# Kernel optimization log

Hardware: AMD Instinct MI355X
Metric: run time of the kernel (lower is better)

The kernel has to match this reference:

```python
import jax, jax.numpy as jnp
import numpy as np

HIDDEN = 1024
NUM_HEAD = 16
HEAD_DIM = HIDDEN // NUM_HEAD
VOCAB = 32000
MAX_LEN = 1024
EMBED = 512
BATCH = 4
SEQ = MAX_LEN  # mask broadcasting requires seq == max_len


def setup_inputs() -> dict:
    key = jax.random.key(0)
    ks = jax.random.split(key, 12)
    std = 0.02
    inp = {
        'input_ids': jax.random.randint(ks[0], (BATCH, SEQ), 0, VOCAB),
        'W_word': jax.random.normal(ks[1], (VOCAB, EMBED), jnp.float32) * std,
        'W_pos': jax.random.normal(ks[2], (MAX_LEN, EMBED), jnp.float32) * std,
        'Wq': jax.random.normal(ks[3], (HIDDEN, HIDDEN), jnp.float32) * std,
        'Wk': jax.random.normal(ks[4], (HIDDEN, HIDDEN), jnp.float32) * std,
        'Wv': jax.random.normal(ks[5], (HIDDEN, HIDDEN), jnp.float32) * std,
        'Wo': jax.random.normal(ks[6], (HIDDEN, HIDDEN), jnp.float32) * std,
        'W1': jax.random.normal(ks[7], (4 * HIDDEN, HIDDEN), jnp.float32) * std,
        'W2': jax.random.normal(ks[8], (HIDDEN, 4 * HIDDEN), jnp.float32) * std,
        'W_eh': jax.random.normal(ks[9], (HIDDEN, EMBED), jnp.float32) * std,
        'W_he': jax.random.normal(ks[10], (EMBED, HIDDEN), jnp.float32) * std,
        'W_lm': jax.random.normal(ks[11], (VOCAB, EMBED), jnp.float32) * std,
    }
    return inp


def reference(input_ids, W_word, W_pos, Wq, Wk, Wv, Wo, W1, W2, W_eh, W_he, W_lm):
    B, S = input_ids.shape
    # embeddings
    h = W_word[input_ids] + W_pos[jnp.arange(S)][None, :, :]  # [B,S,E]
    h = h @ W_eh.T  # embed -> hidden, [B,S,H]
    residual = h
    # QKV projections (Linear with weight [out,in]: y = x @ W.T)
    q = (h @ Wq.T).reshape(B, S, NUM_HEAD, HEAD_DIM).transpose(0, 2, 1, 3)
    k = (h @ Wk.T).reshape(B, S, NUM_HEAD, HEAD_DIM).transpose(0, 2, 1, 3)
    v = (h @ Wv.T).reshape(B, S, NUM_HEAD, HEAD_DIM).transpose(0, 2, 1, 3)
    # note: original scales by sqrt(hidden_size), NOT sqrt(head_dim)
    scores = jnp.einsum('bhqd,bhkd->bhqk', q, k) / jnp.sqrt(jnp.float32(HIDDEN))
    mask = jnp.tril(jnp.ones((S, S), dtype=bool))[None, None]
    scores = jnp.where(mask, scores, jnp.finfo(jnp.float32).min)
    attn = jax.nn.softmax(scores.astype(jnp.float32), axis=-1)
    out = jnp.einsum('bhqk,bhkd->bhqd', attn, v)
    out = out.transpose(0, 2, 1, 3).reshape(B, S, HIDDEN)
    h = residual + out @ Wo.T
    # MLP
    residual = h
    x = jax.nn.relu(h @ W1.T)
    h = residual + x @ W2.T
    # hidden -> embed, lm head
    h = h @ W_he.T
    logits = h @ W_lm.T  # [B,S,VOCAB]
    return logits
```

## Files before the change

### kernel.cpp

```cpp
#include <hip/hip_runtime.h>
#include <hip/hip_bf16.h>

#define HIDDEN 1024
#define NHEAD 16
#define HDIM 64
#define VOCAB 32000
#define SEQLEN 1024
#define EMBED 512
#define BATCH 4
#define ROWS (BATCH*SEQLEN)

typedef __bf16 bf16x8 __attribute__((ext_vector_type(8)));
typedef float f32x4 __attribute__((ext_vector_type(4)));
typedef unsigned short u16;

#define MFMA(a_, b_, c_) __builtin_amdgcn_mfma_f32_16x16x32_bf16(a_, b_, c_, 0, 0, 0)

#define VMCNT4 asm volatile("s_waitcnt vmcnt(4)" ::: "memory")
#define VMCNT0 asm volatile("s_waitcnt vmcnt(0)" ::: "memory")
#define LGKM0  asm volatile("s_waitcnt lgkmcnt(0)" ::: "memory")
#define CFENCE asm volatile("" ::: "memory")
#define SBAR   __builtin_amdgcn_s_barrier()
#define SCHEDB __builtin_amdgcn_sched_barrier(0)

__device__ __forceinline__ u16 f2bf(float f) {
  unsigned u = __builtin_bit_cast(unsigned, f);
  u = u + 0x7FFFu + ((u >> 16) & 1u);
  return (u16)(u >> 16);
}
__device__ __forceinline__ float bf2f(u16 s) {
  unsigned u = (unsigned)s << 16;
  return __builtin_bit_cast(float, u);
}

#define GLDS(g_, l_) __builtin_amdgcn_global_load_lds( \
    (const __attribute__((address_space(1))) void*)(g_), \
    (__attribute__((address_space(3))) void*)(l_), 16, 0, 0)

struct Prep {
  const float* src[8]; u16* dst[8];
  const float* wlm; u16* wlm_dst;
  const int* ids; const float* wword; const float* wpos; u16* h0b;
};
__global__ void prep_kernel(Prep pp) {
  int b = blockIdx.x;
  if (b < 13312) {
    int seg, off;
    if (b < 4096)        { seg = b >> 10; off = b & 1023; }
    else if (b < 8192)   { seg = 4; off = b - 4096; }
    else if (b < 12288)  { seg = 5; off = b - 8192; }
    else if (b < 12800)  { seg = 6; off = b - 12288; }
    else                 { seg = 7; off = b - 12800; }
    size_t i = ((size_t)off * 256 + threadIdx.x) * 4;
    float4 v = *(const float4*)(pp.src[seg] + i);
    unsigned a = f2bf(v.x) | ((unsigned)f2bf(v.y) << 16);
    unsigned d = f2bf(v.z) | ((unsigned)f2bf(v.w) << 16);
    *(uint2*)(pp.dst[seg] + i) = make_uint2(a, d);
  } else if (b < 29312) {
    if (!pp.wlm_dst) return;
    int off = b - 13312;
    size_t i = ((size_t)off * 256 + threadIdx.x) * 4;
    float4 v = *(const float4*)(pp.wlm + i);
    unsigned a = f2bf(v.x) | ((unsigned)f2bf(v.y) << 16);
    unsigned d = f2bf(v.z) | ((unsigned)f2bf(v.w) << 16);
    *(uint2*)(pp.wlm_dst + i) = make_uint2(a, d);
  } else {
    int off = b - 29312;
    int row = off * 2 + (threadIdx.x >> 7);
    int e = (threadIdx.x & 127) * 4;
    int s = row & (SEQLEN - 1);
    int id = pp.ids[row];
    float4 a = *(const float4*)(pp.wword + (size_t)id * EMBED + e);
    float4 c = *(const float4*)(pp.wpos + (size_t)s * EMBED + e);
    unsigned lo = f2bf(a.x + c.x) | ((unsigned)f2bf(a.y + c.y) << 16);
    unsigned hi = f2bf(a.z + c.z) | ((unsigned)f2bf(a.w + c.w) << 16);
    *(uint2*)(pp.h0b + (size_t)row * EMBED + e) = make_uint2(lo, hi);
  }
}

template<int EPI, bool WF32, bool WB16, bool BF32, bool SWZ, bool NT, int BN>
__global__ __launch_bounds__(256, 2) void gemm128(
    const u16* __restrict__ A, const u16* __restrict__ Bb,
    const float* __restrict__ Bf,
    float* __restrict__ C, u16* __restrict__ Cb,
    const u16* __restrict__ R, int K, int ldc)
{
  constexpr int NF  = BN / 32;
  constexpr int BCH = BN / 32;
  __shared__ __align__(16) u16 smem[16384 + 2 * BN * 64];
  u16* As0 = &smem[0];
  u16* As1 = &smem[8192];
  u16* Bs0 = &smem[16384];
  u16* Bs1 = &smem[16384 + BN * 64];

  int tid = threadIdx.x;
  int lane = tid & 63, wave = tid >> 6;
  int wr = wave >> 1, wc = wave & 1;
  int cl = lane & 15, gp = (lane >> 4) & 3;

  int bx = blockIdx.x, by = blockIdx.y;
  if (SWZ) {
    int nwg = gridDim.x * gridDim.y;
    int flat = by * gridDim.x + bx;
    int cpx = nwg >> 3;
    int swz = (flat & 7) * cpx + (flat >> 3);
    bx = swz % gridDim.x; by = swz / gridDim.x;
  }
  int m0 = bx * 128, n0 = by * BN;

  int srow8 = lane >> 3;
  int scol = (((lane & 7) - srow8) & 7) * 8;
  int pos0 = ((gp + cl) & 7) * 8;
  int pos1 = ((gp + cl + 4) & 7) * 8;

  f32x4 acc[4][NF] = {};
  int nk = K >> 6;

  #pragma unroll
  for (int i = 0; i < 4; ++i) {
    int c = i * 4 + wave;
    GLDS(A + (size_t)(m0 + c * 8 + srow8) * K + scol, As0 + c * 512);
  }
  if (!BF32) {
    #pragma unroll
    for (int i = 0; i < BCH; ++i) {
      int c = i * 4 + wave;
      GLDS(Bb + (size_t)(n0 + c * 8 + srow8) * K + scol, Bs0 + c * 512);
    }
  } else {
    #pragma unroll
    for (int it = 0; it < BN / 32; ++it) {
      int idx = it * 256 + tid;
      int row = idx >> 3, p = idx & 7;
      int gc = (p - row) & 7;
      const float* src = Bf + (size_t)(n0 + row) * K + gc * 8;
      float4 v0 = *(const float4*)src, v1 = *(const float4*)(src + 4);
      union { bf16x8 v; u16 s[8]; } u;
      u.s[0]=f2bf(v0.x); u.s[1]=f2bf(v0.y); u.s[2]=f2bf(v0.z); u.s[3]=f2bf(v0.w);
      u.s[4]=f2bf(v1.x); u.s[5]=f2bf(v1.y); u.s[6]=f2bf(v1.z); u.s[7]=f2bf(v1.w);
      *(bf16x8*)&Bs0[row * 64 + p * 8] = u.v;
    }
  }

  for (int kt = 0; kt < nk; ++kt) {
    int buf = kt & 1;
    u16* Asb = buf ? As1 : As0;
    u16* Bsb = buf ? Bs1 : Bs0;
    u16* Asn = buf ? As0 : As1;
    u16* Bsn = buf ? Bs0 : Bs1;
    int kb = (kt + 1) << 6;
    bool more = kt + 1 < nk;

    if (more) {
      #pragma unroll
      for (int i = 0; i < 4; ++i) {
        int c = i * 4 + wave;
        GLDS(A + (size_t)(m0 + c * 8 + srow8) * K + kb + scol, Asn + c * 512);
      }
    }
    if (BF32) { VMCNT0; } else if (more) { VMCNT4; } else { VMCNT0; }
    SCHEDB;
    SBAR;
    CFENCE; SCHEDB;

    bf16x8 af[4][2], bfv[NF][2];
    #pragma unroll
    for (int n = 0; n < NF; ++n) {
      int r = (wc * (BN / 2) + n * 16 + cl) * 64;
      bfv[n][0] = *(const bf16x8*)&Bsb[r + pos0];
      bfv[n][1] = *(const bf16x8*)&Bsb[r + pos1];
    }
    #pragma unroll
    for (int m = 0; m < 4; ++m) {
      int r = (wr * 64 + m * 16 + cl) * 64;
      af[m][0] = *(const bf16x8*)&Asb[r + pos0];
      af[m][1] = *(const bf16x8*)&Asb[r + pos1];
    }

    __builtin_amdgcn_s_setprio(1);
    #pragma unroll
    for (int m = 0; m < 2; ++m)
      #pragma unroll
      for (int n = 0; n < NF; ++n)
        #pragma unroll
        for (int ks = 0; ks < 2; ++ks)
          acc[m][n] = MFMA(af[m][ks], bfv[n][ks], acc[m][n]);
    __builtin_amdgcn_s_setprio(0);

    if (more) {
      if (!BF32) {
        #pragma unroll
        for (int i = 0; i < BCH; ++i) {
          int c = i * 4 + wave;
          GLDS(Bb + (size_t)(n0 + c * 8 + srow8) * K + kb + scol, Bsn + c * 512);
        }
      } else {
        #pragma unroll
        for (int it = 0; it < BN / 32; ++it) {
          int idx = it * 256 + tid;
          int row = idx >> 3, p = idx & 7;
          int gc = (p - row) & 7;
          const float* src = Bf + (size_t)(n0 + row) * K + kb + gc * 8;
          float4 v0 = *(const float4*)src, v1 = *(const float4*)(src + 4);
          union { bf16x8 v; u16 s[8]; } u;
          u.s[0]=f2bf(v0.x); u.s[1]=f2bf(v0.y); u.s[2]=f2bf(v0.z); u.s[3]=f2bf(v0.w);
          u.s[4]=f2bf(v1.x); u.s[5]=f2bf(v1.y); u.s[6]=f2bf(v1.z); u.s[7]=f2bf(v1.w);
          *(bf16x8*)&Bsn[row * 64 + p * 8] = u.v;
        }
      }
    }

    __builtin_amdgcn_s_setprio(1);
    #pragma unroll
    for (int n = 0; n < NF; ++n)
      #pragma unroll
      for (int ks = 0; ks < 2; ++ks)
        acc[2][n] = MFMA(af[2][ks], bfv[n][ks], acc[2][n]);
    __builtin_amdgcn_s_setprio(0);

    LGKM0;
    SCHEDB;
    SBAR;
    CFENCE; SCHEDB;

    __builtin_amdgcn_s_setprio(1);
    #pragma unroll
    for (int n = 0; n < NF; ++n)
      #pragma unroll
      for (int ks = 0; ks < 2; ++ks)
        acc[3][n] = MFMA(af[3][ks], bfv[n][ks], acc[3][n]);
    __builtin_amdgcn_s_setprio(0);
  }

  if constexpr (WF32 && !WB16 && BN == 128) {
    float* Cst = (float*)&smem[0];
    __syncthreads();
    #pragma unroll
    for (int g = 0; g < 2; ++g) {
      if (wr == g) {
        #pragma unroll
        for (int m = 0; m < 4; ++m)
          #pragma unroll
          for (int n = 0; n < 4; ++n)
            #pragma unroll
            for (int j = 0; j < 4; ++j)
              Cst[(m * 16 + gp * 4 + j) * 132 + wc * 64 + n * 16 + cl] = acc[m][n][j];
      }
      __syncthreads();
      int r2 = lane >> 5, cw = lane & 31;
      #pragma unroll
      for (int p = 0; p < 8; ++p) {
        int r = p * 8 + wave * 2 + r2;
        int grow = m0 + g * 64 + r;
        f32x4 v = *(f32x4*)&Cst[r * 132 + cw * 4];
        if constexpr (EPI == 1) {
          ushort4 rv = *(const ushort4*)&R[(size_t)grow * ldc + n0 + cw * 4];
          v[0] += bf2f(rv.x); v[1] += bf2f(rv.y); v[2] += bf2f(rv.z); v[3] += bf2f(rv.w);
        }
        if constexpr (EPI == 2) {
          #pragma unroll
          for (int j = 0; j < 4; ++j) v[j] = fmaxf(v[j], 0.f);
        }
        if (NT) __builtin_nontemporal_store(v, (f32x4*)&C[(size_t)grow * ldc + n0 + cw * 4]);
        else *(f32x4*)&C[(size_t)grow * ldc + n0 + cw * 4] = v;
      }
      __syncthreads();
    }
  } else {
    int r0 = gp * 4;
    #pragma unroll
    for (int m = 0; m < 4; ++m) {
      #pragma unroll
      for (int n = 0; n < NF; ++n) {
        int col = n0 + wc * (BN / 2) + n * 16 + cl;
        #pragma unroll
        for (int j = 0; j < 4; ++j) {
          int row = m0 + wr * 64 + m * 16 + r0 + j;
          float v = acc[m][n][j];
          if (EPI == 1) v += bf2f(R[(size_t)row * ldc + col]);
          if (EPI == 2) v = fmaxf(v, 0.f);
          if (WF32) C[(size_t)row * ldc + col] = v;
          if (WB16) Cb[(size_t)row * ldc + col] = f2bf(v);
        }
      }
    }
  }
}

template<int EPI, bool WF32, bool WB16, bool SWZ, bool NT = false>
__global__ __launch_bounds__(512) void gemm256(
    const u16* __restrict__ A, const u16* __restrict__ B,
    float* __restrict__ C, u16* __restrict__ Cb,
    const u16* __restrict__ R, int K, int ldc)
{
  __shared__ __align__(16) u16 smem[4][256 * 64];
  int tid = threadIdx.x;
  int lane = tid & 63, wave = tid >> 6;
  int wr = wave >> 2, wc = wave & 3;
  int cl = lane & 15, gp = (lane >> 4) & 3;

  int bx = blockIdx.x, by = blockIdx.y;
  if (SWZ) {
    int nwg = gridDim.x * gridDim.y;
    int flat = by * gridDim.x + bx;
    int cpx = nwg >> 3;
    int swz = (flat & 7) * cpx + (flat >> 3);
    bx = swz % gridDim.x; by = swz / gridDim.x;
  }
  int m0 = bx * 256, n0 = by * 256;

  int srow8 = lane >> 3;
  int scol = (((lane & 7) - srow8) & 7) * 8;
  int pos0 = ((gp + cl) & 7) * 8;
  int pos1 = ((gp + cl + 4) & 7) * 8;

  f32x4 acc[8][4] = {};
  int nk = K >> 6;

  #pragma unroll
  for (int i = 0; i < 4; ++i) {
    int c = i * 8 + wave;
    GLDS(A + (size_t)(m0 + c * 8 + srow8) * K + scol, &smem[0][c * 512]);
  }
  #pragma unroll
  for (int i = 0; i < 4; ++i) {
    int c = i * 8 + wave;
    GLDS(B + (size_t)(n0 + c * 8 + srow8) * K + scol, &smem[2][c * 512]);
  }

  for (int kt = 0; kt < nk; ++kt) {
    int buf = kt & 1;
    int kb = (kt + 1) << 6;
    bool more = kt + 1 < nk;

    if (more) {
      #pragma unroll
      for (int i = 0; i < 4; ++i) {
        int c = i * 8 + wave;
        GLDS(A + (size_t)(m0 + c * 8 + srow8) * K + kb + scol, &smem[buf ^ 1][c * 512]);
      }
      VMCNT4;
    } else {
      VMCNT0;
    }
    SCHEDB;
    SBAR;
    CFENCE; SCHEDB;

    bf16x8 af0[4][2], af1[4][2], bf0[2][2], bf1[2][2];
    #pragma unroll
    for (int n = 0; n < 2; ++n) {
      int r = (wc * 64 + n * 16 + cl) * 64;
      bf0[n][0] = *(const bf16x8*)&smem[2 + buf][r + pos0];
      bf0[n][1] = *(const bf16x8*)&smem[2 + buf][r + pos1];
    }
    #pragma unroll
    for (int m = 0; m < 4; ++m) {
      int r = (wr * 128 + m * 16 + cl) * 64;
      af0[m][0] = *(const bf16x8*)&smem[buf][r + pos0];
      af0[m][1] = *(const bf16x8*)&smem[buf][r + pos1];
    }
    #pragma unroll
    for (int n = 0; n < 2; ++n) {
      int r = (wc * 64 + (n + 2) * 16 + cl) * 64;
      bf1[n][0] = *(const bf16x8*)&smem[2 + buf][r + pos0];
      bf1[n][1] = *(const bf16x8*)&smem[2 + buf][r + pos1];
    }
    #pragma unroll
    for (int m = 0; m < 4; ++m) {
      int r = (wr * 128 + (m + 4) * 16 + cl) * 64;
      af1[m][0] = *(const bf16x8*)&smem[buf][r + pos0];
      af1[m][1] = *(const bf16x8*)&smem[buf][r + pos1];
    }

    __builtin_amdgcn_s_setprio(1);
    #pragma unroll
    for (int m = 0; m < 4; ++m)
      #pragma unroll
      for (int n = 0; n < 2; ++n)
        #pragma unroll
        for (int ks = 0; ks < 2; ++ks)
          acc[m][n] = MFMA(af0[m][ks], bf0[n][ks], acc[m][n]);
    __builtin_amdgcn_s_setprio(0);

    if (more) {
      #pragma unroll
      for (int i = 0; i < 4; ++i) {
        int c = i * 8 + wave;
        GLDS(B + (size_t)(n0 + c * 8 + srow8) * K + kb + scol, &smem[2 + (buf ^ 1)][c * 512]);
      }
    }

    __builtin_amdgcn_s_setprio(1);
    #pragma unroll
    for (int m = 0; m < 4; ++m)
      #pragma unroll
      for (int n = 0; n < 2; ++n)
        #pragma unroll
        for (int ks = 0; ks < 2; ++ks)
          acc[m][n + 2] = MFMA(af0[m][ks], bf1[n][ks], acc[m][n + 2]);
    __builtin_amdgcn_s_setprio(0);

    LGKM0;
    SCHEDB;
    SBAR;
    CFENCE; SCHEDB;

    __builtin_amdgcn_s_setprio(1);
    #pragma unroll
    for (int m = 0; m < 4; ++m)
      #pragma unroll
      for (int n = 0; n < 2; ++n)
        #pragma unroll
        for (int ks = 0; ks < 2; ++ks)
          acc[m + 4][n] = MFMA(af1[m][ks], bf0[n][ks], acc[m + 4][n]);
    #pragma unroll
    for (int m = 0; m < 4; ++m)
      #pragma unroll
      for (int n = 0; n < 2; ++n)
        #pragma unroll
        for (int ks = 0; ks < 2; ++ks)
          acc[m + 4][n + 2] = MFMA(af1[m][ks], bf1[n][ks], acc[m + 4][n + 2]);
    __builtin_amdgcn_s_setprio(0);
  }

  if constexpr (WF32 && !WB16) {
    float* Cst = (float*)&smem[0][0];
    __syncthreads();
    #pragma unroll
    for (int g = 0; g < 4; ++g) {
      if ((g >> 1) == wr) {
        #pragma unroll
        for (int k = 0; k < 4; ++k) {
          int ar = (g & 1) * 4 + k;
          int rl = ar * 16 + gp * 4 - (g & 1) * 64;
          #pragma unroll
          for (int n = 0; n < 4; ++n) {
            int col = wc * 64 + n * 16 + cl;
            #pragma unroll
            for (int j = 0; j < 4; ++j)
              Cst[(rl + j) * 260 + col] = acc[ar][n][j];
          }
        }
      }
      __syncthreads();
      #pragma unroll
      for (int p = 0; p < 8; ++p) {
        int r = p * 8 + wave;
        int c4 = lane * 4;
        int grow = m0 + g * 64 + r;
        f32x4 v = *(f32x4*)&Cst[r * 260 + c4];
        if constexpr (EPI == 1) {
          ushort4 rv = *(const ushort4*)&R[(size_t)grow * ldc + n0 + c4];
          v[0] += bf2f(rv.x); v[1] += bf2f(rv.y); v[2] += bf2f(rv.z); v[3] += bf2f(rv.w);
        }
        if constexpr (EPI == 2) {
          #pragma unroll
          for (int j = 0; j < 4; ++j) v[j] = fmaxf(v[j], 0.f);
        }
        if (NT) __builtin_nontemporal_store(v, (f32x4*)&C[(size_t)grow * ldc + n0 + c4]);
        else *(f32x4*)&C[(size_t)grow * ldc + n0 + c4] = v;
      }
      __syncthreads();
    }
  } else {
    int r0 = gp * 4;
    #pragma unroll
    for (int m = 0; m < 8; ++m) {
      #pragma unroll
      for (int n = 0; n < 4; ++n) {
        int col = n0 + wc * 64 + n * 16 + cl;
        #pragma unroll
        for (int j = 0; j < 4; ++j) {
          int row = m0 + wr * 128 + m * 16 + r0 + j;
          float v = acc[m][n][j];
          if (EPI == 1) v += bf2f(R[(size_t)row * ldc + col]);
          if (EPI == 2) v = fmaxf(v, 0.f);
          if (WF32) C[(size_t)row * ldc + col] = v;
          if (WB16) Cb[(size_t)row * ldc + col] = f2bf(v);
        }
      }
    }
  }
}

#define LSTR 72
__global__ __launch_bounds__(256) void attn_kernel(const u16* __restrict__ qkv,
                                                   u16* __restrict__ outb) {
  __shared__ u16 Ksm[2][64 * 64];
  __shared__ u16 Vsm[2][64 * LSTR];
  __shared__ u16 Psm[64 * LSTR];
  int pi = blockIdx.x, h = blockIdx.y, b = blockIdx.z;
  int qbA = pi, qbB = 15 - pi;
  int tid = threadIdx.x;
  int lane = tid & 63, wave = tid >> 6;
  int cl = lane & 15, gp = lane >> 4;
  int srow8 = lane >> 3;
  int gsrc = (((lane & 7) - srow8) & 7) * 8;

  const u16* base = qkv + (size_t)b * SEQLEN * (3 * HIDDEN);

  bf16x8 qA0, qA1, qB0, qB1;
  {
    const u16* qp = base + (size_t)(qbA * 64 + wave * 16 + cl) * (3 * HIDDEN) + h * HDIM;
    qA0 = *(const bf16x8*)(qp + gp * 8);
    qA1 = *(const bf16x8*)(qp + 32 + gp * 8);
    const u16* qq = base + (size_t)(qbB * 64 + wave * 16 + cl) * (3 * HIDDEN) + h * HDIM;
    qB0 = *(const bf16x8*)(qq + gp * 8);
    qB1 = *(const bf16x8*)(qq + 32 + gp * 8);
  }

  ushort4 vr[4];
  auto stageK = [&](int t, int bb) {
    #pragma unroll
    for (int i = 0; i < 2; ++i) {
      int c = wave * 2 + i;
      int row = c * 8 + srow8;
      GLDS(base + (size_t)(t * 64 + row) * (3 * HIDDEN) + HIDDEN + h * HDIM + gsrc,
           &Ksm[bb][c * 512]);
    }
  };
  auto loadV = [&](int t) {
    #pragma unroll
    for (int it = 0; it < 4; ++it) {
      int idx = it * 256 + tid;
      int row = idx >> 4, c4 = (idx & 15) * 4;
      vr[it] = *(const ushort4*)(base + (size_t)(t * 64 + row) * (3 * HIDDEN) +
                                 2 * HIDDEN + h * HDIM + c4);
    }
  };
  auto writeV = [&](int bb) {
    #pragma unroll
    for (int it = 0; it < 4; ++it) {
      int idx = it * 256 + tid;
      int row = idx >> 4, c4 = (idx & 15) * 4;
      Vsm[bb][(c4 + 0) * LSTR + row] = vr[it].x;
      Vsm[bb][(c4 + 1) * LSTR + row] = vr[it].y;
      Vsm[bb][(c4 + 2) * LSTR + row] = vr[it].z;
      Vsm[bb][(c4 + 3) * LSTR + row] = vr[it].w;
    }
  };

  float mA[4], lA[4], mB[4], lB[4];
  f32x4 oA[4] = {}, oB[4] = {};
  #pragma unroll
  for (int j = 0; j < 4; ++j) { mA[j] = -INFINITY; lA[j] = 0.f; mB[j] = -INFINITY; lB[j] = 0.f; }

  auto stateStep = [&](int t, int buf, int qb, bf16x8 q0, bf16x8 q1,
                       float* mrow, float* lrow, f32x4* oacc) {
    f32x4 sfr[4];
    __builtin_amdgcn_s_setprio(1);
    #pragma unroll
    for (int n = 0; n < 4; ++n) {
      f32x4 z = {};
      bf16x8 kf0 = *(const bf16x8*)&Ksm[buf][(n * 16 + cl) * 64 + ((gp + cl) & 7) * 8];
      bf16x8 kf1 = *(const bf16x8*)&Ksm[buf][(n * 16 + cl) * 64 + ((gp + cl + 4) & 7) * 8];
      z = MFMA(q0, kf0, z);
      z = MFMA(q1, kf1, z);
      sfr[n] = z;
    }
    __builtin_amdgcn_s_setprio(0);

    bool diag = (t == qb);
    #pragma unroll
    for (int n = 0; n < 4; ++n)
      #pragma unroll
      for (int j = 0; j < 4; ++j) {
        float sv = sfr[n][j] * 0.03125f;
        if (diag) {
          int lr = wave * 16 + gp * 4 + j;
          int lc = n * 16 + cl;
          sv = (lc <= lr) ? sv : -1e30f;
        }
        sfr[n][j] = sv;
      }
    float so[4];
    #pragma unroll
    for (int j = 0; j < 4; ++j) {
      float tm = fmaxf(fmaxf(sfr[0][j], sfr[1][j]), fmaxf(sfr[2][j], sfr[3][j]));
      tm = fmaxf(tm, __shfl_xor(tm, 1));
      tm = fmaxf(tm, __shfl_xor(tm, 2));
      tm = fmaxf(tm, __shfl_xor(tm, 4));
      tm = fmaxf(tm, __shfl_xor(tm, 8));
      float mn = fmaxf(mrow[j], tm);
      so[j] = __expf(mrow[j] - mn);
      mrow[j] = mn;
      float ts = 0.f;
      #pragma unroll
      for (int n = 0; n < 4; ++n) {
        float p = __expf(sfr[n][j] - mn);
        sfr[n][j] = p;
        ts += p;
      }
      ts += __shfl_xor(ts, 1); ts += __shfl_xor(ts, 2);
      ts += __shfl_xor(ts, 4); ts += __shfl_xor(ts, 8);
      lrow[j] = lrow[j] * so[j] + ts;
    }
    #pragma unroll
    for (int n = 0; n < 4; ++n)
      #pragma unroll
      for (int j = 0; j < 4; ++j)
        oacc[n][j] *= so[j];

    #pragma unroll
    for (int n = 0; n < 4; ++n)
      #pragma unroll
      for (int j = 0; j < 4; ++j)
        Psm[(wave * 16 + gp * 4 + j) * LSTR + n * 16 + cl] = f2bf(sfr[n][j]);
    __builtin_amdgcn_sched_barrier(0);

    bf16x8 pa0 = *(const bf16x8*)&Psm[(wave * 16 + cl) * LSTR + gp * 8];
    bf16x8 pa1 = *(const bf16x8*)&Psm[(wave * 16 + cl) * LSTR + 32 + gp * 8];
    __builtin_amdgcn_s_setprio(1);
    #pragma unroll
    for (int n = 0; n < 4; ++n) {
      bf16x8 vb0 = *(const bf16x8*)&Vsm[buf][(n * 16 + cl) * LSTR + gp * 8];
      bf16x8 vb1 = *(const bf16x8*)&Vsm[buf][(n * 16 + cl) * LSTR + 32 + gp * 8];
      oacc[n] = MFMA(pa0, vb0, oacc[n]);
      oacc[n] = MFMA(pa1, vb1, oacc[n]);
    }
    __builtin_amdgcn_s_setprio(0);
  };

  stageK(0, 0);
  loadV(0);
  writeV(0);
  __syncthreads();

  for (int t = 0; t <= qbB; ++t) {
    int buf = t & 1;
    bool more = t < qbB;
    if (more) { stageK(t + 1, buf ^ 1); loadV(t + 1); }

    stateStep(t, buf, qbB, qB0, qB1, mB, lB, oB);
    if (more) writeV(buf ^ 1);
    if (t <= qbA)
      stateStep(t, buf, qbA, qA0, qA1, mA, lA, oA);

    __syncthreads();
  }

  #pragma unroll
  for (int n = 0; n < 4; ++n)
    #pragma unroll
    for (int j = 0; j < 4; ++j) {
      int lr = wave * 16 + gp * 4 + j;
      int d = n * 16 + cl;
      outb[(size_t)(b * SEQLEN + qbA * 64 + lr) * HIDDEN + h * HDIM + d] = f2bf(oA[n][j] / lA[j]);
      outb[(size_t)(b * SEQLEN + qbB * 64 + lr) * HIDDEN + h * HDIM + d] = f2bf(oB[n][j] / lB[j]);
    }
}

extern "C" void kernel_launch(void* const* d_in, const int* in_sizes, int n_in,
                              void* d_out, int out_size, void* d_ws, size_t ws_size,
                              hipStream_t stream) {
  const int*   ids    = (const int*)d_in[0];
  const float* W_word = (const float*)d_in[1];
  const float* W_pos  = (const float*)d_in[2];
  const float* Wq     = (const float*)d_in[3];
  const float* Wk     = (const float*)d_in[4];
  const float* Wv     = (const float*)d_in[5];
  const float* Wo     = (const float*)d_in[6];
  const float* W1     = (const float*)d_in[7];
  const float* W2     = (const float*)d_in[8];
  const float* W_eh   = (const float*)d_in[9];
  const float* W_he   = (const float*)d_in[10];
  const float* W_lm   = (const float*)d_in[11];
  float* out = (float*)d_out;
  char*  ob  = (char*)d_out;
  char*  wb  = (char*)d_ws;

  const size_t MB = 1024 * 1024;
  u16*   h0b   = (u16*)(ob + 32 * MB);
  u16*   h1b   = (u16*)(ob + 36 * MB);
  u16*   qkvb  = (u16*)(ob + 44 * MB);
  u16*   attnb = (u16*)(ob + 68 * MB);
  u16*   h2b   = (u16*)(ob + 76 * MB);
  u16*   xb    = (u16*)(ob + 84 * MB);
  u16*   h3b   = (u16*)(ob + 116 * MB);
  u16*   Wqkv_b= (u16*)(ob + 124 * MB);
  u16*   Wo_b  = (u16*)(ob + 130 * MB);
  u16*   W1_b  = (u16*)(ob + 132 * MB);
  u16*   W2_b  = (u16*)(ob + 140 * MB);
  u16*   Weh_b = (u16*)(ob + 148 * MB);
  u16*   Whe_b = (u16*)(ob + 149 * MB);
  u16*   he_b  = (u16*)(wb + 0);
  u16*   Wlm_b = (u16*)(wb + 4 * MB);
  bool big_ws = ws_size >= 36 * MB;

  Prep pp;
  pp.src[0] = Wq;  pp.dst[0] = Wqkv_b + 0 * 1024 * 1024;
  pp.src[1] = Wk;  pp.dst[1] = Wqkv_b + 1 * 1024 * 1024;
  pp.src[2] = Wv;  pp.dst[2] = Wqkv_b + 2 * 1024 * 1024;
  pp.src[3] = Wo;  pp.dst[3] = Wo_b;
  pp.src[4] = W1;  pp.dst[4] = W1_b;
  pp.src[5] = W2;  pp.dst[5] = W2_b;
  pp.src[6] = W_eh; pp.dst[6] = Weh_b;
  pp.src[7] = W_he; pp.dst[7] = Whe_b;
  pp.wlm = W_lm; pp.wlm_dst = big_ws ? Wlm_b : nullptr;
  pp.ids = ids; pp.wword = W_word; pp.wpos = W_pos; pp.h0b = h0b;
  prep_kernel<<<dim3(31360), 256, 0, stream>>>(pp);

  gemm128<0, false, true, false, false, false, 128><<<dim3(32, 8), 256, 0, stream>>>(
      h0b, Weh_b, nullptr, nullptr, h1b, nullptr, 512, HIDDEN);
  gemm128<0, false, true, false, false, false, 128><<<dim3(32, 24), 256, 0, stream>>>(
      h1b, Wqkv_b, nullptr, nullptr, qkvb, nullptr, 1024, 3 * HIDDEN);
  attn_kernel<<<dim3(8, 16, 4), 256, 0, stream>>>(qkvb, attnb);
  gemm128<1, false, true, false, false, false, 128><<<dim3(32, 8), 256, 0, stream>>>(
      attnb, Wo_b, nullptr, nullptr, h2b, h1b, 1024, HIDDEN);
  gemm256<2, false, true, false><<<dim3(16, 16), 512, 0, stream>>>(
      h2b, W1_b, nullptr, xb, nullptr, 1024, 4 * HIDDEN);
  gemm128<1, false, true, false, false, false, 128><<<dim3(32, 8), 256, 0, stream>>>(
      xb, W2_b, nullptr, nullptr, h3b, h2b, 4096, HIDDEN);
  gemm128<0, false, true, false, false, false, 64><<<dim3(32, 8), 256, 0, stream>>>(
      h3b, Whe_b, nullptr, nullptr, he_b, nullptr, 1024, EMBED);
  if (big_ws)
    gemm256<0, true, false, true, true><<<dim3(16, 125), 512, 0, stream>>>(
        he_b, Wlm_b, out, nullptr, nullptr, 512, VOCAB);
  else
    gemm128<0, true, false, true, true, true, 128><<<dim3(32, 250), 256, 0, stream>>>(
        he_b, nullptr, W_lm, out, nullptr, nullptr, 512, VOCAB);
}
```

Measured before the change: 416.0 us.

## Restructure gemm256 pipeline into quarter-tile staged loads with deeper prefetch

Splits each K-tile's A/B shared-memory load into four half-tile stages and issues them interleaved across the four MFMA phases of the previous tile, keeping about seven stages in flight with vmcnt(6) waits. The aim is smoother overlap of global-to-LDS traffic with matrix math and lower stall per barrier. It also adds a launch bound of two blocks per CU, which constrains register allocation. More barriers per iteration and the register cap may add overhead or spills.

```diff
diff --git a/kernel.cpp b/kernel.cpp
--- a/kernel.cpp
+++ b/kernel.cpp
@@ -16,6 +16,7 @@
 
 #define MFMA(a_, b_, c_) __builtin_amdgcn_mfma_f32_16x16x32_bf16(a_, b_, c_, 0, 0, 0)
 
+#define VMCNT6 asm volatile("s_waitcnt vmcnt(6)" ::: "memory")
 #define VMCNT4 asm volatile("s_waitcnt vmcnt(4)" ::: "memory")
 #define VMCNT0 asm volatile("s_waitcnt vmcnt(0)" ::: "memory")
 #define LGKM0  asm volatile("s_waitcnt lgkmcnt(0)" ::: "memory")
@@ -288,12 +289,12 @@
 }
 
 template<int EPI, bool WF32, bool WB16, bool SWZ, bool NT = false>
-__global__ __launch_bounds__(512) void gemm256(
+__global__ __launch_bounds__(512, 2) void gemm256(
     const u16* __restrict__ A, const u16* __restrict__ B,
     float* __restrict__ C, u16* __restrict__ Cb,
     const u16* __restrict__ R, int K, int ldc)
 {
-  __shared__ __align__(16) u16 smem[4][256 * 64];
+  __shared__ __align__(16) u16 smem[2][32768];
   int tid = threadIdx.x;
   int lane = tid & 63, wave = tid >> 6;
   int wr = wave >> 2, wc = wave & 3;
@@ -316,96 +317,95 @@
 
   f32x4 acc[8][4] = {};
   int nk = K >> 6;
-
-  #pragma unroll
-  for (int i = 0; i < 4; ++i) {
-    int c = i * 8 + wave;
-    GLDS(A + (size_t)(m0 + c * 8 + srow8) * K + scol, &smem[0][c * 512]);
-  }
-  #pragma unroll
-  for (int i = 0; i < 4; ++i) {
-    int c = i * 8 + wave;
-    GLDS(B + (size_t)(n0 + c * 8 + srow8) * K + scol, &smem[2][c * 512]);
-  }
-
-  for (int kt = 0; kt < nk; ++kt) {
-    int buf = kt & 1;
-    int kb = (kt + 1) << 6;
-    bool more = kt + 1 < nk;
-
-    if (more) {
-      #pragma unroll
-      for (int i = 0; i < 4; ++i) {
-        int c = i * 8 + wave;
-        GLDS(A + (size_t)(m0 + c * 8 + srow8) * K + kb + scol, &smem[buf ^ 1][c * 512]);
-      }
-      VMCNT4;
-    } else {
-      VMCNT0;
-    }
-    SCHEDB;
-    SBAR;
-    CFENCE; SCHEDB;
-
+  int hmax = nk << 2;
+
+  auto stageH = [&](int h) {
+    if (h >= hmax) return;
+    int tau = h >> 2, s = h & 3;
+    int high = (s & 1) ? 128 : 0;
+    int boff = ((s < 2) ? 16384 : 0) + ((s & 1) ? 8192 : 0);
+    const u16* src = (s < 2) ? B : A;
+    int g0 = ((s < 2) ? n0 : m0) + high;
+    int kb = tau << 6;
+    #pragma unroll
+    for (int i = 0; i < 2; ++i) {
+      int c = wave * 2 + i;
+      GLDS(src + (size_t)(g0 + c * 8 + srow8) * K + kb + scol,
+           &smem[tau & 1][boff + c * 512]);
+    }
+  };
+
+  for (int h = 0; h < 7; ++h) stageH(h);
+  VMCNT6;
+  SCHEDB; CFENCE;
+  SBAR;
+  CFENCE;
+
+  for (int t = 0; t < nk; ++t) {
+    const u16* Ab = &smem[t & 1][0];
+    const u16* Bb2 = &smem[t & 1][16384];
+    int p0 = t << 2;
     bf16x8 af0[4][2], af1[4][2], bf0[2][2], bf1[2][2];
+
     #pragma unroll
     for (int n = 0; n < 2; ++n) {
       int r = (wc * 64 + n * 16 + cl) * 64;
-      bf0[n][0] = *(const bf16x8*)&smem[2 + buf][r + pos0];
-      bf0[n][1] = *(const bf16x8*)&smem[2 + buf][r + pos1];
+      bf0[n][0] = *(const bf16x8*)&Bb2[r + pos0];
+      bf0[n][1] = *(const bf16x8*)&Bb2[r + pos1];
+    }
+    #pragma unroll
+    for (int n = 0; n < 2; ++n) {
+      int r = (wc * 64 + (n + 2) * 16 + cl) * 64;
+      bf1[n][0] = *(const bf16x8*)&Bb2[r + pos0];
+      bf1[n][1] = *(const bf16x8*)&Bb2[r + pos1];
     }
     #pragma unroll
     for (int m = 0; m < 4; ++m) {
       int r = (wr * 128 + m * 16 + cl) * 64;
-      af0[m][0] = *(const bf16x8*)&smem[buf][r + pos0];
-      af0[m][1] = *(const bf16x8*)&smem[buf][r + pos1];
-    }
-    #pragma unroll
-    for (int n = 0; n < 2; ++n) {
-      int r = (wc * 64 + (n + 2) * 16 + cl) * 64;
-      bf1[n][0] = *(const bf16x8*)&smem[2 + buf][r + pos0];
-      bf1[n][1] = *(const bf16x8*)&smem[2 + buf][r + pos1];
-    }
+      af0[m][0] = *(const bf16x8*)&Ab[r + pos0];
+      af0[m][1] = *(const bf16x8*)&Ab[r + pos1];
+    }
+    stageH(p0 + 7);
+    CFENCE;
+    SBAR;
+    LGKM0; SCHEDB;
+    __builtin_amdgcn_s_setprio(1);
+    #pragma unroll
+    for (int m = 0; m < 4; ++m)
+      #pragma unroll
+      for (int n = 0; n < 2; ++n)
+        #pragma unroll
+        for (int ks = 0; ks < 2; ++ks)
+          acc[m][n] = MFMA(af0[m][ks], bf0[n][ks], acc[m][n]);
+    __builtin_amdgcn_s_setprio(0);
+    CFENCE;
+    SBAR;
+
+    stageH(p0 + 8);
+    CFENCE;
+    SBAR;
+    __builtin_amdgcn_s_setprio(1);
+    #pragma unroll
+    for (int m = 0; m < 4; ++m)
+      #pragma unroll
+      for (int n = 0; n < 2; ++n)
+        #pragma unroll
+        for (int ks = 0; ks < 2; ++ks)
+          acc[m][n + 2] = MFMA(af0[m][ks], bf1[n][ks], acc[m][n + 2]);
+    __builtin_amdgcn_s_setprio(0);
+    CFENCE;
+    SBAR;
+
     #pragma unroll
     for (int m = 0; m < 4; ++m) {
       int r = (wr * 128 + (m + 4) * 16 + cl) * 64;
-      af1[m][0] = *(const bf16x8*)&smem[buf][r + pos0];
-      af1[m][1] = *(const bf16x8*)&smem[buf][r + pos1];
-    }
-
-    __builtin_amdgcn_s_setprio(1);
-    #pragma unroll
-    for (int m = 0; m < 4; ++m)
-      #pragma unroll
-      for (int n = 0; n < 2; ++n)
-        #pragma unroll
-        for (int ks = 0; ks < 2; ++ks)
-          acc[m][n] = MFMA(af0[m][ks], bf0[n][ks], acc[m][n]);
-    __builtin_amdgcn_s_setprio(0);
-
-    if (more) {
-      #pragma unroll
-      for (int i = 0; i < 4; ++i) {
-        int c = i * 8 + wave;
-        GLDS(B + (size_t)(n0 + c * 8 + srow8) * K + kb + scol, &smem[2 + (buf ^ 1)][c * 512]);
-      }
-    }
-
-    __builtin_amdgcn_s_setprio(1);
-    #pragma unroll
-    for (int m = 0; m < 4; ++m)
-      #pragma unroll
-      for (int n = 0; n < 2; ++n)
-        #pragma unroll
-        for (int ks = 0; ks < 2; ++ks)
-          acc[m][n + 2] = MFMA(af0[m][ks], bf1[n][ks], acc[m][n + 2]);
-    __builtin_amdgcn_s_setprio(0);
-
-    LGKM0;
-    SCHEDB;
-    SBAR;
-    CFENCE; SCHEDB;
-
+      af1[m][0] = *(const bf16x8*)&Ab[r + pos0];
+      af1[m][1] = *(const bf16x8*)&Ab[r + pos1];
+    }
+    stageH(p0 + 9);
+    CFENCE;
+    SBAR;
+    LGKM0; SCHEDB;
     __builtin_amdgcn_s_setprio(1);
     #pragma unroll
     for (int m = 0; m < 4; ++m)
@@ -414,6 +414,12 @@
         #pragma unroll
         for (int ks = 0; ks < 2; ++ks)
           acc[m + 4][n] = MFMA(af1[m][ks], bf0[n][ks], acc[m + 4][n]);
+    __builtin_amdgcn_s_setprio(0);
+    CFENCE;
+    SBAR;
+
+    stageH(p0 + 10);
+    __builtin_amdgcn_s_setprio(1);
     #pragma unroll
     for (int m = 0; m < 4; ++m)
       #pragma unroll
@@ -422,6 +428,12 @@
         for (int ks = 0; ks < 2; ++ks)
           acc[m + 4][n + 2] = MFMA(af1[m][ks], bf1[n][ks], acc[m + 4][n + 2]);
     __builtin_amdgcn_s_setprio(0);
+    if (t + 1 < nk) {
+      if (t + 2 == nk) { VMCNT0; } else { VMCNT6; }
+    }
+    SCHEDB; CFENCE;
+    SBAR;
+    CFENCE;
   }
 
   if constexpr (WF32 && !WB16) {
```

After: 434.4 us. +4.4%, slower.
